# Optimization experiments

Hardware: AMD Instinct MI355X
Metric: run time of the kernel (lower is better)

Reference implementation:

```python
import jax, jax.numpy as jnp
import numpy as np

N_QUBITS = 10
BATCH = 16384
Q_DEPTH = 2


def _apply_1q_shared(state, U, q):
    # state: [B, 2, 2, ..., 2]; U: [2, 2] complex, acting on wire q
    state = jnp.moveaxis(state, 1 + q, -1)
    state = jnp.einsum('b...i,ji->b...j', state, U)
    return jnp.moveaxis(state, -1, 1 + q)


def _apply_ry_batched(state, angles, q):
    # per-sample RY(angle) on wire q; angles: [B] float
    c = jnp.cos(angles * 0.5).astype(jnp.complex64)
    s = jnp.sin(angles * 0.5).astype(jnp.complex64)
    U = jnp.stack([jnp.stack([c, -s], -1), jnp.stack([s, c], -1)], -2)  # [B,2,2]
    state = jnp.moveaxis(state, 1 + q, -1)
    state = jnp.einsum('b...i,bji->b...j', state, U)
    return jnp.moveaxis(state, -1, 1 + q)


def _rot_matrix(phi, theta, omega):
    # PennyLane Rot = RZ(omega) @ RY(theta) @ RZ(phi)
    c = jnp.cos(theta * 0.5)
    s = jnp.sin(theta * 0.5)
    m00 = jnp.exp(-0.5j * (phi + omega)) * c
    m01 = -jnp.exp(0.5j * (phi - omega)) * s
    m10 = jnp.exp(-0.5j * (phi - omega)) * s
    m11 = jnp.exp(0.5j * (phi + omega)) * c
    return jnp.stack([jnp.stack([m00, m01]), jnp.stack([m10, m11])]).astype(jnp.complex64)


def _apply_cnot(state, c, t):
    st = jnp.moveaxis(state, (1 + c, 1 + t), (1, 2))  # [B, ctrl, tgt, ...]
    st = jnp.stack([st[:, 0], st[:, 1, ::-1]], axis=1)  # flip target where ctrl=1
    return jnp.moveaxis(st, (1, 2), (1 + c, 1 + t))


def setup_inputs() -> dict:
    key = jax.random.key(0)
    k1, k2 = jax.random.split(key)
    x = jax.random.uniform(k1, (BATCH, N_QUBITS), dtype=jnp.float32) * np.pi
    q_weights = 0.01 * jax.random.normal(k2, (Q_DEPTH, N_QUBITS, 3), dtype=jnp.float32)
    return {"x": x, "q_weights": q_weights}


def reference(x, q_weights) -> jnp.ndarray:
    B, n = x.shape
    L = q_weights.shape[0]
    # |0...0> statevector, batched: [B] + [2]*n (axis q <-> wire q, wire 0 most significant)
    state = jnp.zeros((B, 2 ** n), jnp.complex64).at[:, 0].set(1.0)
    state = state.reshape((B,) + (2,) * n)
    # AngleEmbedding(rotation='Y')
    for q in range(n):
        state = _apply_ry_batched(state, x[:, q], q)
    # StronglyEntanglingLayers: Rot on each wire, then ring of CNOTs with range (l % (n-1)) + 1
    for l in range(L):
        for q in range(n):
            U = _rot_matrix(q_weights[l, q, 0], q_weights[l, q, 1], q_weights[l, q, 2])
            state = _apply_1q_shared(state, U, q)
        r = (l % (n - 1)) + 1
        for q in range(n):
            state = _apply_cnot(state, q, (q + r) % n)
    probs = jnp.abs(state.reshape(B, 2 ** n)) ** 2  # [B, 2^n]
    bits = (np.arange(2 ** n)[:, None] >> (n - 1 - np.arange(n))[None, :]) & 1
    signs = jnp.asarray(1.0 - 2.0 * bits, jnp.float32)  # [2^n, n], PauliZ eigenvalues
    return (probs @ signs).astype(jnp.float32)  # [B, n] expvals
```

## Files before the change

### kernel.cpp

```cpp
#include <hip/hip_runtime.h>

#define DEVINL __device__ __forceinline__

typedef float f32x2 __attribute__((ext_vector_type(2)));

struct GC { int laneXor, regXor, rowL, rowR; };
struct Circ { GC g[20]; int sgnL[10], sgnR[10]; };

constexpr Circ build_circ() {
    Circ c{};
    unsigned A[10] = {};
    for (int i = 0; i < 10; ++i) A[i] = 1u << i;
    for (int w = 0; w < 10; ++w) {
        int pos = 9 - w;
        unsigned m = 1u << pos;
        c.g[w] = GC{ int(m >> 5), int(m & 31u), int(m >> 5), int(m & 31u) };
    }
    for (int q = 0; q < 10; ++q) { int pc = 9 - q, pt = 9 - ((q + 1) % 10); A[pt] ^= A[pc]; }
    unsigned M[10] = {}, Inv[10] = {};
    for (int i = 0; i < 10; ++i) { M[i] = A[i]; Inv[i] = 1u << i; }
    for (int col = 0; col < 10; ++col) {
        int piv = col;
        while (!((M[piv] >> col) & 1u)) ++piv;
        unsigned tm = M[col]; M[col] = M[piv]; M[piv] = tm;
        unsigned ti = Inv[col]; Inv[col] = Inv[piv]; Inv[piv] = ti;
        for (int r = 0; r < 10; ++r)
            if (r != col && ((M[r] >> col) & 1u)) { M[r] ^= M[col]; Inv[r] ^= Inv[col]; }
    }
    for (int w = 0; w < 10; ++w) {
        int pos = 9 - w;
        unsigned m = 0;
        for (int i = 0; i < 10; ++i) m |= ((Inv[i] >> pos) & 1u) << i;
        unsigned row = A[pos];
        c.g[10 + w] = GC{ int(m >> 5), int(m & 31u), int(row >> 5), int(row & 31u) };
    }
    for (int q = 0; q < 10; ++q) { int pc = 9 - q, pt = 9 - ((q + 2) % 10); A[pt] ^= A[pc]; }
    for (int q = 0; q < 10; ++q) { unsigned row = A[9 - q]; c.sgnL[q] = int(row >> 5); c.sgnR[q] = int(row & 31u); }
    return c;
}

constexpr Circ CC = build_circ();

static_assert(CC.g[10].laneXor == 24 && CC.g[10].regXor == 0,  "w0 m");
static_assert(CC.g[11].laneXor == 12 && CC.g[11].regXor == 0,  "w1 m");
static_assert(CC.g[12].laneXor == 6  && CC.g[12].regXor == 0,  "w2 m");
static_assert(CC.g[13].laneXor == 3  && CC.g[13].regXor == 0,  "w3 m");
static_assert(CC.g[14].laneXor == 1  && CC.g[14].regXor == 16, "w4 m");
static_assert(CC.g[15].laneXor == 0  && CC.g[15].regXor == 24, "w5 m");
static_assert(CC.g[16].laneXor == 0  && CC.g[16].regXor == 12, "w6 m");
static_assert(CC.g[17].laneXor == 0  && CC.g[17].regXor == 6,  "w7 m");
static_assert(CC.g[18].laneXor == 0  && CC.g[18].regXor == 3,  "w8 m");
static_assert(CC.g[19].laneXor == 24 && CC.g[19].regXor == 1,  "w9 m");
static_assert(CC.g[10].rowL == 15 && CC.g[10].rowR == 31, "w0 row");
static_assert(CC.g[11].rowL == 24 && CC.g[11].rowR == 0,  "w1 row");
static_assert(CC.g[12].rowL == 28 && CC.g[12].rowR == 0,  "w2 row");
static_assert(CC.g[13].rowL == 30 && CC.g[13].rowR == 0,  "w3 row");
static_assert(CC.g[14].rowL == 31 && CC.g[14].rowR == 0,  "w4 row");
static_assert(CC.g[15].rowL == 31 && CC.g[15].rowR == 16, "w5 row");
static_assert(CC.g[16].rowL == 31 && CC.g[16].rowR == 24, "w6 row");
static_assert(CC.g[17].rowL == 31 && CC.g[17].rowR == 28, "w7 row");
static_assert(CC.g[18].rowL == 31 && CC.g[18].rowR == 30, "w8 row");
static_assert(CC.g[19].rowL == 31 && CC.g[19].rowR == 31, "w9 row");

DEVINL float csw(float v, int sw) {
    return __int_as_float(__float_as_int(v) ^ sw);
}

template<int XOR>
DEVINL float fetch(float v, int lane) {
    if constexpr (XOR == 0)      return v;
    else if constexpr (XOR == 1) return __int_as_float(__builtin_amdgcn_update_dpp(0, __float_as_int(v), 0xB1, 0xF, 0xF, true));
    else if constexpr (XOR == 2) return __int_as_float(__builtin_amdgcn_update_dpp(0, __float_as_int(v), 0x4E, 0xF, 0xF, true));
    else if constexpr (XOR == 3) return __int_as_float(__builtin_amdgcn_update_dpp(0, __float_as_int(v), 0x1B, 0xF, 0xF, true));
    else                         return __int_as_float(__builtin_amdgcn_ds_swizzle(__float_as_int(v), 0x1F | (XOR << 10)));
}

DEVINL void pk_fma_acc(f32x2& a, f32x2 t, f32x2 b) {
    asm("v_pk_fma_f32 %0, %1, %2, %0" : "+v"(a) : "v"(t), "v"(b));
}

DEVINL f32x2 cmul(f32x2 a, f32x2 b) {
    f32x2 r;
    r.x = a.x * b.x - a.y * b.y;
    r.y = a.x * b.y + a.y * b.x;
    return r;
}

__device__ __attribute__((aligned(16))) float g_cst[80];

__global__ void qprep(const float* __restrict__ qw) {
    int g = threadIdx.x;
    if (g < 10) {
        float phi = qw[g * 3 + 0], th = qw[g * 3 + 1], om = qw[g * 3 + 2];
        float c = cosf(0.5f * th), s = sinf(0.5f * th);
        float apo = 0.5f * (phi + om), amo = 0.5f * (phi - om);
        g_cst[g * 4 + 0] =  cosf(apo) * c;
        g_cst[g * 4 + 1] = -sinf(apo) * c;
        g_cst[g * 4 + 2] = -cosf(amo) * s;
        g_cst[g * 4 + 3] = -sinf(amo) * s;
    } else if (g < 20) {
        int w = g - 10;
        float phi = qw[g * 3 + 0], th = qw[g * 3 + 1];
        float c = cosf(0.5f * th), s = sinf(0.5f * th);
        g_cst[40 + w] = s / c;
        g_cst[50 + w * 2 + 0] =  cosf(0.5f * phi);
        g_cst[50 + w * 2 + 1] = -sinf(0.5f * phi);
    } else if (g == 20) {
        float p = 1.f;
        for (int w = 0; w < 10; ++w) p *= cosf(0.5f * qw[(10 + w) * 3 + 1]);
        g_cst[70] = p;
    }
}

DEVINL void wf(const float* cst, float xw, int w, f32x2& f0, f32x2& f1) {
    float h = 0.5f * xw;
    float s = __sinf(h), c = __cosf(h);
    float m0 = cst[w * 4 + 0], m1 = cst[w * 4 + 1], m2 = cst[w * 4 + 2], m3 = cst[w * 4 + 3];
    f0.x =  m0 * c + m2 * s;
    f0.y =  m1 * c + m3 * s;
    f1.x = -m2 * c + m0 * s;
    f1.y =  m3 * c - m1 * s;
}

template<int W>
DEVINL void apply_gate(f32x2 (&a2)[32], const float* cst, int lane, const int (&sw)[10]) {
    constexpr GC gc = CC.g[10 + W];
    float tt = csw(cst[40 + W], sw[W]);
    f32x2 tp; tp.x = tt;  tp.y = tt;
    f32x2 tn; tn.x = -tt; tn.y = -tt;
    if constexpr (gc.laneXor == 0) {
        #pragma unroll
        for (int r = 0; r < 32; ++r) {
            const int r2 = r ^ gc.regXor;
            if (r < r2) {
                f32x2 old = a2[r];
                const bool sR  = __builtin_popcount(unsigned(gc.rowR & r )) & 1;
                const bool sR2 = __builtin_popcount(unsigned(gc.rowR & r2)) & 1;
                pk_fma_acc(a2[r],  sR  ? tp : tn, a2[r2]);
                pk_fma_acc(a2[r2], sR2 ? tp : tn, old);
            }
        }
    } else {
        #pragma unroll
        for (int c = 0; c < 2; ++c) {
            f32x2 b2[16];
            #pragma unroll
            for (int i = 0; i < 16; ++i) {
                const int r = (i & 7) + c * 8 + ((i >> 3) << 4);
                f32x2 s = a2[r ^ gc.regXor];
                b2[i].x = fetch<gc.laneXor>(s.x, lane);
                b2[i].y = fetch<gc.laneXor>(s.y, lane);
            }
            #pragma unroll
            for (int i = 0; i < 16; ++i) {
                const int r = (i & 7) + c * 8 + ((i >> 3) << 4);
                const bool sR = __builtin_popcount(unsigned(gc.rowR & r)) & 1;
                pk_fma_acc(a2[r], sR ? tp : tn, b2[i]);
            }
        }
    }
}

__global__ __launch_bounds__(256) void qsim(const float* __restrict__ x,
                                            float* __restrict__ out, int B) {
    const float* cst = g_cst;
    int lane = threadIdx.x & 63;
    int l5 = lane & 31;
    int b = blockIdx.x * 8 + (threadIdx.x >> 5);
    if (b >= B) return;
    const float* xb = x + b * 10;

    int p24 = (l5 >> 4) ^ (l5 >> 3);
    int p28 = p24 ^ (l5 >> 2);
    int p30 = p28 ^ (l5 >> 1);
    int p31 = p30 ^ l5;
    int p15 = p31 ^ (l5 >> 4);
    int s24 = p24 << 31, s28 = p28 << 31, s30 = p30 << 31,
        s31 = p31 << 31, s15 = p15 << 31;
    int sw_[10] = { s15, s24, s28, s30, s31, s31, s31, s31, s31, s31 };

    f32x2 t01[4], t23[4], f5t[2];
    {
        f32x2 a0, a1, b0, b1;
        wf(cst, xb[9], 9, a0, a1);
        wf(cst, xb[8], 8, b0, b1);
        t01[0] = cmul(a0, b0); t01[1] = cmul(a1, b0);
        t01[2] = cmul(a0, b1); t01[3] = cmul(a1, b1);
        wf(cst, xb[7], 7, a0, a1);
        wf(cst, xb[6], 6, b0, b1);
        t23[0] = cmul(a0, b0); t23[1] = cmul(a1, b0);
        t23[2] = cmul(a0, b1); t23[3] = cmul(a1, b1);
        wf(cst, xb[5], 5, f5t[0], f5t[1]);
    }

    f32x2 E0; E0.x = cst[50];      E0.y = csw(cst[51], s15);
    f32x2 E1; E1.x = cst[52];      E1.y = csw(cst[53], s24);
    f32x2 E2; E2.x = cst[54];      E2.y = csw(cst[55], s28);
    f32x2 E3; E3.x = cst[56];      E3.y = csw(cst[57], s30);
    f32x2 E4; E4.x = cst[58];      E4.y = csw(cst[59], s31);
    f32x2 E5; E5.x = cst[60];      E5.y = csw(cst[61], s31);
    f32x2 E6; E6.x = cst[62];      E6.y = csw(cst[63], s31);
    f32x2 E7; E7.x = cst[64];      E7.y = csw(cst[65], s31);
    f32x2 E8; E8.x = cst[66];      E8.y = csw(cst[67], s31);
    f32x2 E9; E9.x = cst[68];      E9.y = csw(cst[69], s31);

    f32x2 lf;
    {
        f32x2 ea = cmul(cmul(E1, E2), cmul(E3, E4));
        float sc = cst[70];
        lf.x = ea.x * sc; lf.y = ea.y * sc;
        #pragma unroll
        for (int jj = 0; jj < 5; ++jj) {
            int w = 4 - jj;
            f32x2 f0, f1;
            wf(cst, xb[w], w, f0, f1);
            int bit = (l5 >> jj) & 1;
            f32x2 p; p.x = bit ? f1.x : f0.x; p.y = bit ? f1.y : f0.y;
            lf = cmul(lf, p);
        }
    }

    f32x2 f5p[2];
    f5p[0] = cmul(f5t[0], E5);
    { f32x2 e5c; e5c.x = E5.x; e5c.y = -E5.y; f5p[1] = cmul(f5t[1], e5c); }
    f32x2 V00 = cmul(E6, E7);
    f32x2 V01; { f32x2 e7c; e7c.x = E7.x; e7c.y = -E7.y; V01 = cmul(E6, e7c); }
    f32x2 EB = cmul(E9, E0);
    f32x2 H0 = cmul(E8, EB);
    f32x2 H1; { f32x2 ebc; ebc.x = EB.x; ebc.y = -EB.y; H1 = cmul(E8, ebc); }

    f32x2 tf[8];
    #pragma unroll
    for (int j = 0; j < 8; ++j) {
        f32x2 tA = cmul(t23[j & 3], f5p[j >> 2]);
        const int s6 = ((j >> 2) ^ (j >> 1)) & 1;
        const int s7 = s6 ^ (j & 1);
        f32x2 V;
        V.x = s6 ? (s7 ? V00.x : V01.x) : (s7 ? V01.x : V00.x);
        V.y = s6 ? -(s7 ? V00.y : V01.y) : (s7 ? V01.y : V00.y);
        tf[j] = cmul(tA, V);
    }

    f32x2 g4[4];
    #pragma unroll
    for (int v = 0; v < 4; ++v) g4[v] = cmul(lf, t01[v]);
    f32x2 a2[32];
    #pragma unroll
    for (int r = 0; r < 32; ++r) {
        f32x2 t = cmul(g4[r & 3], tf[(r >> 2) & 7]);
        f32x2 G;
        G.x = (r & 1) ? H1.x : H0.x;
        G.y = (r & 1) ? H1.y : H0.y;
        if (__builtin_popcount(unsigned(r & 30)) & 1) G.y = -G.y;
        a2[r] = cmul(t, G);
    }

    apply_gate<0>(a2, cst, lane, sw_);
    apply_gate<5>(a2, cst, lane, sw_);
    apply_gate<1>(a2, cst, lane, sw_);
    apply_gate<3>(a2, cst, lane, sw_);
    apply_gate<2>(a2, cst, lane, sw_);
    apply_gate<6>(a2, cst, lane, sw_);
    apply_gate<9>(a2, cst, lane, sw_);
    apply_gate<4>(a2, cst, lane, sw_);
    apply_gate<7>(a2, cst, lane, sw_);
    apply_gate<8>(a2, cst, lane, sw_);

    float wv[32];
    #pragma unroll
    for (int r = 0; r < 32; ++r) wv[r] = a2[r].x * a2[r].x + a2[r].y * a2[r].y;
    #pragma unroll
    for (int bS = 1; bS < 16; bS <<= 1) {
        #pragma unroll
        for (int r = 0; r < 32; ++r) {
            if (!(r & bS)) {
                float xv = wv[r], yv = wv[r | bS];
                wv[r]      = xv + yv;
                wv[r | bS] = xv - yv;
            }
        }
    }

    float e[10];
    #pragma unroll
    for (int q = 0; q < 10; ++q) {
        const int R = CC.sgnR[q];
        float num = (R & 16) ? (wv[R ^ 16] - wv[R]) : (wv[R] + wv[R ^ 16]);
        int slq = __popc(unsigned(l5 & CC.sgnL[q])) & 1;
        e[q] = csw(num, slq << 31);
    }

    #pragma unroll
    for (int q = 0; q < 10; ++q) {
        e[q] += fetch<1>(e[q], lane);
        e[q] += fetch<2>(e[q], lane);
    }
    int s = l5 & 3;
    bool s1 = (s & 1) != 0, s2 = (s & 2) != 0;
    float v0 = s1 ? e[1] : e[0];
    float u0 = s1 ? e[3] : e[2];
    v0 = s2 ? u0 : v0;
    float v1 = s1 ? e[5] : e[4];
    float u1 = s1 ? e[7] : e[6];
    v1 = s2 ? u1 : v1;
    float v2 = s1 ? e[9] : e[8];

    v0 += fetch<4>(v0, lane);   v1 += fetch<4>(v1, lane);   v2 += fetch<4>(v2, lane);
    v0 += fetch<8>(v0, lane);   v1 += fetch<8>(v1, lane);   v2 += fetch<8>(v2, lane);
    v0 += fetch<16>(v0, lane);  v1 += fetch<16>(v1, lane);  v2 += fetch<16>(v2, lane);

    float vo = v0;
    int hi = l5 >> 2;
    vo = (hi == 1) ? v1 : vo;
    vo = (hi == 2) ? v2 : vo;
    if (l5 < 10) out[b * 10 + l5] = vo;
}

extern "C" void kernel_launch(void* const* d_in, const int* in_sizes, int n_in,
                              void* d_out, int out_size, void* d_ws, size_t ws_size,
                              hipStream_t stream) {
    const float* x  = (const float*)d_in[0];
    const float* qw = (const float*)d_in[1];
    float* out = (float*)d_out;
    int B = in_sizes[0] / 10;
    int blocks = (B + 7) / 8;
    hipLaunchKernelGGL(qprep, dim3(1), dim3(64), 0, stream, qw);
    hipLaunchKernelGGL(qsim, dim3(blocks), dim3(256), 0, stream, x, out, B);
}
```

Measured before the change: 82.09 us.

## Relabel lane basis so second-layer gate partners use cheap DPP exchanges

```diff
diff --git a/kernel.cpp b/kernel.cpp
--- a/kernel.cpp
+++ b/kernel.cpp
@@ -5,7 +5,7 @@
 typedef float f32x2 __attribute__((ext_vector_type(2)));
 
 struct GC { int laneXor, regXor, rowL, rowR; };
-struct Circ { GC g[20]; int sgnL[10], sgnR[10]; };
+struct Circ { GC g[20]; int sgnL[10], sgnR[10]; int lsel[5]; };
 
 constexpr Circ build_circ() {
     Circ c{};
@@ -36,31 +36,69 @@
     }
     for (int q = 0; q < 10; ++q) { int pc = 9 - q, pt = 9 - ((q + 2) % 10); A[pt] ^= A[pc]; }
     for (int q = 0; q < 10; ++q) { unsigned row = A[9 - q]; c.sgnL[q] = int(row >> 5); c.sgnR[q] = int(row & 31u); }
+
+    unsigned Ucols[5] = {};
+    {
+        unsigned tgt[5] = {16, 8, 7, 2, 1};
+        unsigned acc = 0;
+        for (int k = 0; k < 5; ++k) { acc ^= tgt[k]; Ucols[k] = acc; }
+    }
+    unsigned Urows[5] = {};
+    for (int r = 0; r < 5; ++r)
+        for (int cc = 0; cc < 5; ++cc)
+            Urows[r] |= ((Ucols[cc] >> r) & 1u) << cc;
+    unsigned MM[5] = {}, AI[5] = {};
+    for (int i = 0; i < 5; ++i) { MM[i] = Urows[i]; AI[i] = 1u << i; }
+    for (int col = 0; col < 5; ++col) {
+        int piv = col;
+        while (!((MM[piv] >> col) & 1u)) ++piv;
+        unsigned tm = MM[col]; MM[col] = MM[piv]; MM[piv] = tm;
+        unsigned ti = AI[col]; AI[col] = AI[piv]; AI[piv] = ti;
+        for (int r = 0; r < 5; ++r)
+            if (r != col && ((MM[r] >> col) & 1u)) { MM[r] ^= MM[col]; AI[r] ^= AI[col]; }
+    }
+    for (int w = 0; w < 10; ++w) {
+        unsigned mL = unsigned(c.g[10 + w].laneXor);
+        unsigned nm = 0;
+        for (int i = 0; i < 5; ++i) if ((mL >> i) & 1u) nm ^= Ucols[i];
+        c.g[10 + w].laneXor = int(nm);
+        unsigned rL = unsigned(c.g[10 + w].rowL);
+        unsigned nr = 0;
+        for (int i = 0; i < 5; ++i) if ((rL >> i) & 1u) nr ^= AI[i];
+        c.g[10 + w].rowL = int(nr);
+    }
+    for (int q = 0; q < 10; ++q) {
+        unsigned sL = unsigned(c.sgnL[q]);
+        unsigned ns = 0;
+        for (int i = 0; i < 5; ++i) if ((sL >> i) & 1u) ns ^= AI[i];
+        c.sgnL[q] = int(ns);
+    }
+    for (int o = 0; o < 5; ++o) c.lsel[o] = int(AI[o]);
     return c;
 }
 
 constexpr Circ CC = build_circ();
 
-static_assert(CC.g[10].laneXor == 24 && CC.g[10].regXor == 0,  "w0 m");
-static_assert(CC.g[11].laneXor == 12 && CC.g[11].regXor == 0,  "w1 m");
-static_assert(CC.g[12].laneXor == 6  && CC.g[12].regXor == 0,  "w2 m");
-static_assert(CC.g[13].laneXor == 3  && CC.g[13].regXor == 0,  "w3 m");
-static_assert(CC.g[14].laneXor == 1  && CC.g[14].regXor == 16, "w4 m");
-static_assert(CC.g[15].laneXor == 0  && CC.g[15].regXor == 24, "w5 m");
-static_assert(CC.g[16].laneXor == 0  && CC.g[16].regXor == 12, "w6 m");
-static_assert(CC.g[17].laneXor == 0  && CC.g[17].regXor == 6,  "w7 m");
-static_assert(CC.g[18].laneXor == 0  && CC.g[18].regXor == 3,  "w8 m");
-static_assert(CC.g[19].laneXor == 24 && CC.g[19].regXor == 1,  "w9 m");
-static_assert(CC.g[10].rowL == 15 && CC.g[10].rowR == 31, "w0 row");
-static_assert(CC.g[11].rowL == 24 && CC.g[11].rowR == 0,  "w1 row");
-static_assert(CC.g[12].rowL == 28 && CC.g[12].rowR == 0,  "w2 row");
-static_assert(CC.g[13].rowL == 30 && CC.g[13].rowR == 0,  "w3 row");
-static_assert(CC.g[14].rowL == 31 && CC.g[14].rowR == 0,  "w4 row");
-static_assert(CC.g[15].rowL == 31 && CC.g[15].rowR == 16, "w5 row");
-static_assert(CC.g[16].rowL == 31 && CC.g[16].rowR == 24, "w6 row");
-static_assert(CC.g[17].rowL == 31 && CC.g[17].rowR == 28, "w7 row");
-static_assert(CC.g[18].rowL == 31 && CC.g[18].rowR == 30, "w8 row");
-static_assert(CC.g[19].rowL == 31 && CC.g[19].rowR == 31, "w9 row");
+static_assert(CC.g[10].laneXor == 1  && CC.g[10].regXor == 0,  "w0");
+static_assert(CC.g[11].laneXor == 2  && CC.g[11].regXor == 0,  "w1");
+static_assert(CC.g[12].laneXor == 7  && CC.g[12].regXor == 0,  "w2");
+static_assert(CC.g[13].laneXor == 8  && CC.g[13].regXor == 0,  "w3");
+static_assert(CC.g[14].laneXor == 16 && CC.g[14].regXor == 16, "w4");
+static_assert(CC.g[15].laneXor == 0  && CC.g[15].regXor == 24, "w5");
+static_assert(CC.g[16].laneXor == 0  && CC.g[16].regXor == 12, "w6");
+static_assert(CC.g[17].laneXor == 0  && CC.g[17].regXor == 6,  "w7");
+static_assert(CC.g[18].laneXor == 0  && CC.g[18].regXor == 3,  "w8");
+static_assert(CC.g[19].laneXor == 1  && CC.g[19].regXor == 1,  "w9");
+static_assert(CC.g[10].rowR == 31, "w0 rowR");
+static_assert(CC.g[11].rowR == 0,  "w1 rowR");
+static_assert(CC.g[12].rowR == 0,  "w2 rowR");
+static_assert(CC.g[13].rowR == 0,  "w3 rowR");
+static_assert(CC.g[14].rowR == 0,  "w4 rowR");
+static_assert(CC.g[15].rowR == 16, "w5 rowR");
+static_assert(CC.g[16].rowR == 24, "w6 rowR");
+static_assert(CC.g[17].rowR == 28, "w7 rowR");
+static_assert(CC.g[18].rowR == 30, "w8 rowR");
+static_assert(CC.g[19].rowR == 31, "w9 rowR");
 
 DEVINL float csw(float v, int sw) {
     return __int_as_float(__float_as_int(v) ^ sw);
@@ -72,6 +110,8 @@
     else if constexpr (XOR == 1) return __int_as_float(__builtin_amdgcn_update_dpp(0, __float_as_int(v), 0xB1, 0xF, 0xF, true));
     else if constexpr (XOR == 2) return __int_as_float(__builtin_amdgcn_update_dpp(0, __float_as_int(v), 0x4E, 0xF, 0xF, true));
     else if constexpr (XOR == 3) return __int_as_float(__builtin_amdgcn_update_dpp(0, __float_as_int(v), 0x1B, 0xF, 0xF, true));
+    else if constexpr (XOR == 7) return __int_as_float(__builtin_amdgcn_update_dpp(0, __float_as_int(v), 0x141, 0xF, 0xF, true));
+    else if constexpr (XOR == 8) return __int_as_float(__builtin_amdgcn_update_dpp(0, __float_as_int(v), 0x128, 0xF, 0xF, true));
     else                         return __int_as_float(__builtin_amdgcn_ds_swizzle(__float_as_int(v), 0x1F | (XOR << 10)));
 }
 
@@ -170,14 +210,10 @@
     if (b >= B) return;
     const float* xb = x + b * 10;
 
-    int p24 = (l5 >> 4) ^ (l5 >> 3);
-    int p28 = p24 ^ (l5 >> 2);
-    int p30 = p28 ^ (l5 >> 1);
-    int p31 = p30 ^ l5;
-    int p15 = p31 ^ (l5 >> 4);
-    int s24 = p24 << 31, s28 = p28 << 31, s30 = p30 << 31,
-        s31 = p31 << 31, s15 = p15 << 31;
-    int sw_[10] = { s15, s24, s28, s30, s31, s31, s31, s31, s31, s31 };
+    int sw_[10];
+    #pragma unroll
+    for (int w = 0; w < 10; ++w)
+        sw_[w] = (__popc(unsigned(l5 & CC.g[10 + w].rowL)) & 1) << 31;
 
     f32x2 t01[4], t23[4], f5t[2];
     {
@@ -193,16 +229,16 @@
         wf(cst, xb[5], 5, f5t[0], f5t[1]);
     }
 
-    f32x2 E0; E0.x = cst[50];      E0.y = csw(cst[51], s15);
-    f32x2 E1; E1.x = cst[52];      E1.y = csw(cst[53], s24);
-    f32x2 E2; E2.x = cst[54];      E2.y = csw(cst[55], s28);
-    f32x2 E3; E3.x = cst[56];      E3.y = csw(cst[57], s30);
-    f32x2 E4; E4.x = cst[58];      E4.y = csw(cst[59], s31);
-    f32x2 E5; E5.x = cst[60];      E5.y = csw(cst[61], s31);
-    f32x2 E6; E6.x = cst[62];      E6.y = csw(cst[63], s31);
-    f32x2 E7; E7.x = cst[64];      E7.y = csw(cst[65], s31);
-    f32x2 E8; E8.x = cst[66];      E8.y = csw(cst[67], s31);
-    f32x2 E9; E9.x = cst[68];      E9.y = csw(cst[69], s31);
+    f32x2 E0; E0.x = cst[50];      E0.y = csw(cst[51], sw_[0]);
+    f32x2 E1; E1.x = cst[52];      E1.y = csw(cst[53], sw_[1]);
+    f32x2 E2; E2.x = cst[54];      E2.y = csw(cst[55], sw_[2]);
+    f32x2 E3; E3.x = cst[56];      E3.y = csw(cst[57], sw_[3]);
+    f32x2 E4; E4.x = cst[58];      E4.y = csw(cst[59], sw_[4]);
+    f32x2 E5; E5.x = cst[60];      E5.y = csw(cst[61], sw_[5]);
+    f32x2 E6; E6.x = cst[62];      E6.y = csw(cst[63], sw_[6]);
+    f32x2 E7; E7.x = cst[64];      E7.y = csw(cst[65], sw_[7]);
+    f32x2 E8; E8.x = cst[66];      E8.y = csw(cst[67], sw_[8]);
+    f32x2 E9; E9.x = cst[68];      E9.y = csw(cst[69], sw_[9]);
 
     f32x2 lf;
     {
@@ -214,7 +250,7 @@
             int w = 4 - jj;
             f32x2 f0, f1;
             wf(cst, xb[w], w, f0, f1);
-            int bit = (l5 >> jj) & 1;
+            int bit = __popc(unsigned(l5 & CC.lsel[jj])) & 1;
             f32x2 p; p.x = bit ? f1.x : f0.x; p.y = bit ? f1.y : f0.y;
             lf = cmul(lf, p);
         }
@@ -255,16 +291,16 @@
         a2[r] = cmul(t, G);
     }
 
+    apply_gate<4>(a2, cst, lane, sw_);
+    apply_gate<5>(a2, cst, lane, sw_);
     apply_gate<0>(a2, cst, lane, sw_);
-    apply_gate<5>(a2, cst, lane, sw_);
+    apply_gate<6>(a2, cst, lane, sw_);
     apply_gate<1>(a2, cst, lane, sw_);
+    apply_gate<7>(a2, cst, lane, sw_);
+    apply_gate<2>(a2, cst, lane, sw_);
+    apply_gate<8>(a2, cst, lane, sw_);
     apply_gate<3>(a2, cst, lane, sw_);
-    apply_gate<2>(a2, cst, lane, sw_);
-    apply_gate<6>(a2, cst, lane, sw_);
     apply_gate<9>(a2, cst, lane, sw_);
-    apply_gate<4>(a2, cst, lane, sw_);
-    apply_gate<7>(a2, cst, lane, sw_);
-    apply_gate<8>(a2, cst, lane, sw_);
 
     float wv[32];
     #pragma unroll
```

Result: slower. 84.56 us (+3.0%).
